# Optimization experiments

Measured on AMD Instinct MI355X. Metric: run time of the kernel, lower is better.

## Reference

```python
import jax, jax.numpy as jnp
import numpy as np

D = 64        # d_model = input_dims
S = 300       # patch_length
DFF = 256     # dff (H feature dim)
NH = 2        # num_heads
DK = D // NH  # 32


def _ln(x, g, b, eps=1e-5):
    m = x.mean(-1, keepdims=True)
    v = ((x - m) ** 2).mean(-1, keepdims=True)
    return (x - m) * jax.lax.rsqrt(v + eps) * g + b


def setup_inputs() -> dict:
    key = jax.random.key(0)
    ks = jax.random.split(key, 20)
    B = 256
    inp = {
        "state": jax.random.normal(ks[0], (B, S, D), dtype=jnp.float32),
        "H": jax.random.normal(ks[1], (B, S, DFF), dtype=jnp.float32),
    }
    # Linear weights stored as [in, out] (torch stores [out, in]; math is x @ W_in_out + b)
    def lin(k, din, dout):
        k1, k2 = jax.random.split(k)
        w = jax.random.normal(k1, (din, dout), dtype=jnp.float32) / np.sqrt(din)
        b = jax.random.normal(k2, (dout,), dtype=jnp.float32) * 0.01
        return w, b
    inp["Wq"], inp["bq"] = lin(ks[2], D, D)
    inp["Wk"], inp["bk"] = lin(ks[3], D, D)
    inp["Wv"], inp["bv"] = lin(ks[4], D, D)
    inp["Wcq"], inp["bcq"] = lin(ks[5], DFF, D)
    inp["Wck"], inp["bck"] = lin(ks[6], DFF, D)
    inp["Wcv"], inp["bcv"] = lin(ks[7], DFF, D)
    # six LayerNorms on d_model (QE/KE/VE from state branch, QH/KH/VH from H branch)
    for name in ["QE", "KE", "VE", "QH", "KH", "VH"]:
        inp[f"g{name}"] = jnp.ones((D,), jnp.float32)
        inp[f"beta{name}"] = jnp.zeros((D,), jnp.float32)
    inp["W1"], inp["b1"] = lin(ks[8], D, 4 * D)
    inp["W2"], inp["b2"] = lin(ks[9], 4 * D, D)
    inp["g1"] = jnp.ones((D,), jnp.float32)   # norm1
    inp["beta1"] = jnp.zeros((D,), jnp.float32)
    return inp


def reference(state, H, Wq, bq, Wk, bk, Wv, bv, Wcq, bcq, Wck, bck, Wcv, bcv,
              gQE, betaQE, gKE, betaKE, gVE, betaVE,
              gQH, betaQH, gKH, betaKH, gVH, betaVH,
              W1, b1, W2, b2, g1, beta1):
    B = state.shape[0]
    # gated q/k/v: LN(Linear(state)) * LN(Linear(H)), split into heads
    def branch(Wx, bx, gx, bbx, Wh, bh, gh, bbh):
        e = _ln(state @ Wx + bx, gx, bbx)
        h = _ln(H @ Wh + bh, gh, bbh)
        return (e * h).reshape(B, S, NH, DK).transpose(0, 2, 1, 3)  # [B,NH,S,DK]
    q = branch(Wq, bq, gQE, betaQE, Wcq, bcq, gQH, betaQH)
    k = branch(Wk, bk, gKE, betaKE, Wck, bck, gKH, betaKH)
    v = branch(Wv, bv, gVE, betaVE, Wcv, bcv, gVH, betaVH)
    scores = jnp.einsum("bhqd,bhkd->bhqk", q, k) / jnp.sqrt(jnp.float32(DK))
    attn = jax.nn.softmax(scores, axis=-1)
    out = jnp.einsum("bhqk,bhkd->bhqd", attn, v)
    out = out.transpose(0, 2, 1, 3).reshape(B, S, NH * DK)
    Z1 = state + out                      # dropout p=0.01 -> identity in eval
    Z2 = _ln(Z1, g1, beta1)
    Z3 = jax.nn.gelu(Z2 @ W1 + b1, approximate=False)  # torch F.gelu default = exact erf
    Z4 = Z3 @ W2 + b2
    return Z1 + Z4
```

## Files before the change

### kernel.cpp

```cpp
#include <hip/hip_runtime.h>
#include <math.h>

namespace {

constexpr int SEQ  = 300;
constexpr int DM   = 64;
constexpr int DFFN = 256;
constexpr int NBAT = 256;
constexpr int ROWS = NBAT * SEQ;
constexpr float EPS = 1e-5f;

typedef __attribute__((ext_vector_type(8))) short s16x8;
typedef __attribute__((ext_vector_type(4))) float f32x4;

__device__ __forceinline__ float4 ld4(const float* p) { return *reinterpret_cast<const float4*>(p); }

__device__ __forceinline__ ushort f2bf(float x) {
  unsigned u = __builtin_bit_cast(unsigned, x);
  u += 0x7FFFu + ((u >> 16) & 1u);
  return (ushort)(u >> 16);
}

struct PrepArgs {
  const float *Wq,*Wk,*Wv,*Wcq,*Wck,*Wcv;
  const float *bq,*bk,*bv,*bcq,*bck,*bcv;
  const float *gQE,*betaQE,*gKE,*betaKE,*gVE,*betaVE;
  const float *gQH,*betaQH,*gKH,*betaKH,*gVH,*betaVH;
  const float *W1,*W2;
  ushort *Bqkv, *W1t, *W2t;
  float *pk;
};

__global__ __launch_bounds__(256) void tb_prep(PrepArgs P) {
  const int idx = blockIdx.x * 256 + threadIdx.x;
  if (idx < 61440) {
    const int c = idx / 12288, rem = idx % 12288;
    const int n = rem >> 6, k = rem & 63;
    const int br = n >> 6, col = n & 63;
    float v;
    if (c == 0) {
      const float* W = (br == 0) ? P.Wq : (br == 1) ? P.Wk : P.Wv;
      v = W[k * DM + col];
    } else {
      const float* W = (br == 0) ? P.Wcq : (br == 1) ? P.Wck : P.Wcv;
      v = W[((c - 1) * 64 + k) * DM + col];
    }
    P.Bqkv[c * 12288 + ((n * 128 + ((k * 2) ^ ((n & 7) << 4))) >> 1)] = f2bf(v);
  } else if (idx < 77824) {
    const int r = idx - 61440, n = r >> 6, k = r & 63;
    P.W1t[(n * 128 + ((k * 2) ^ ((n & 7) << 4))) >> 1] = f2bf(P.W1[k * DFFN + n]);
  } else if (idx < 94208) {
    const int j = idx - 77824;
    const int fragId = j >> 9, within = j & 511;
    const int lane = within >> 3, e = within & 7;
    const int ps = fragId >> 2, nt2 = fragId & 3;
    const int n = nt2 * 16 + (lane & 15);
    const int k = ps * 32 + ((e >> 2) << 4) + ((lane >> 4) << 2) + (e & 3);
    P.W2t[j] = f2bf(P.W2[k * DM + n]);
  } else if (idx < 95360) {
    const int r = idx - 94208, which = r / 192, j = r % 192;
    const int br = j >> 6, col = j & 63;
    const float* s;
    switch (which) {
      case 0:  s = (br==0)?P.bq   :(br==1)?P.bk    :P.bv;     break;
      case 1:  s = (br==0)?P.bcq  :(br==1)?P.bck   :P.bcv;    break;
      case 2:  s = (br==0)?P.gQE  :(br==1)?P.gKE   :P.gVE;    break;
      case 3:  s = (br==0)?P.betaQE:(br==1)?P.betaKE:P.betaVE; break;
      case 4:  s = (br==0)?P.gQH  :(br==1)?P.gKH   :P.gVH;    break;
      default: s = (br==0)?P.betaQH:(br==1)?P.betaKH:P.betaVH; break;
    }
    P.pk[which * 192 + j] = s[col];
  }
}

struct QkvArgs {
  const float *state, *H;
  const ushort *Bqkv;
  const float *pk;
  ushort *qo, *ko, *vo;
};

__global__ __launch_bounds__(256) void tb_qkv(QkvArgs A) {
  __shared__ __align__(16) ushort Ab[4608];
  __shared__ __align__(16) ushort Bb[12288];
  const int t = threadIdx.x;
  const int lane = t & 63, w = t >> 6;
  const int lo = lane & 15, hi = lane >> 4;
  const int rowbase = blockIdx.x * 64;

  f32x4 accE[12], accH[12];
  #pragma unroll
  for (int nt = 0; nt < 12; ++nt) {
    const float bE = A.pk[nt * 16 + lo], bH = A.pk[192 + nt * 16 + lo];
    accE[nt] = (f32x4){bE, bE, bE, bE};
    accH[nt] = (f32x4){bH, bH, bH, bH};
  }

  const int arow = w * 16 + lo;
  const int aswz = (lo & 7) << 4;

#define STAGE_B(c)                                                            \
  _Pragma("unroll")                                                           \
  for (int i = 0; i < 6; ++i) {                                               \
    const int s_ = i * 256 + t;                                               \
    *(uint4*)&Bb[s_ * 8] = *(const uint4*)&A.Bqkv[(c) * 12288 + s_ * 8];      \
  }

#define STAGE_A(SRC, STRIDE)                                                  \
  _Pragma("unroll")                                                           \
  for (int i = 0; i < 4; ++i) {                                               \
    const int p_ = i * 256 + t;                                               \
    const int row_ = p_ >> 4, slot_ = p_ & 15;                                \
    const float4 f_ = ld4(&(SRC)[row_ * (STRIDE) + slot_ * 4]);               \
    ushort4 u_;                                                               \
    u_.x = f2bf(f_.x); u_.y = f2bf(f_.y); u_.z = f2bf(f_.z); u_.w = f2bf(f_.w);\
    *(ushort4*)((char*)Ab + (row_ * 128 + ((slot_ * 8) ^ ((row_ & 7) << 4)))) = u_; \
  }

#define COMPUTE(ACC)                                                          \
  _Pragma("unroll")                                                           \
  for (int ks = 0; ks < 2; ++ks) {                                            \
    const s16x8 af = *(const s16x8*)((const char*)Ab +                        \
        (arow * 128 + ((ks * 64 + hi * 16) ^ aswz)));                         \
    _Pragma("unroll")                                                         \
    for (int nt = 0; nt < 12; ++nt) {                                         \
      const int n_ = nt * 16 + lo;                                            \
      const s16x8 bf = *(const s16x8*)((const char*)Bb +                      \
          (n_ * 128 + ((ks * 64 + hi * 16) ^ ((n_ & 7) << 4))));              \
      ACC[nt] = __builtin_amdgcn_mfma_f32_16x16x32_bf16(af, bf, ACC[nt], 0, 0, 0); \
    }                                                                         \
  }

  STAGE_B(0)
  STAGE_A(A.state + (size_t)rowbase * 64, 64)
  __syncthreads();
  COMPUTE(accE)
  for (int c = 1; c < 5; ++c) {
    __syncthreads();
    STAGE_B(c)
    const float* hsrc = A.H + (size_t)rowbase * 256 + (c - 1) * 64;
    STAGE_A(hsrc, 256)
    __syncthreads();
    COMPUTE(accH)
  }
#undef STAGE_B
#undef STAGE_A
#undef COMPUTE

  const float* gE  = A.pk + 384;
  const float* bEt = A.pk + 576;
  const float* gH  = A.pk + 768;
  const float* bHt = A.pk + 960;
  const int growbase = rowbase + w * 16 + hi * 4;
  float vout[4][4];

  #pragma unroll
  for (int br = 0; br < 3; ++br) {
    #pragma unroll
    for (int r = 0; r < 4; ++r) {
      float s1 = 0.f, s2 = 0.f, u1 = 0.f, u2 = 0.f;
      #pragma unroll
      for (int qq = 0; qq < 4; ++qq) {
        const float ev = accE[br * 4 + qq][r], hv = accH[br * 4 + qq][r];
        s1 += ev; s2 += ev * ev; u1 += hv; u2 += hv * hv;
      }
      #pragma unroll
      for (int m = 1; m <= 8; m <<= 1) {
        s1 += __shfl_xor(s1, m, 64); s2 += __shfl_xor(s2, m, 64);
        u1 += __shfl_xor(u1, m, 64); u2 += __shfl_xor(u2, m, 64);
      }
      const float me = s1 * (1.f / 64.f);
      const float re = rsqrtf(s2 * (1.f / 64.f) - me * me + EPS);
      const float mh = u1 * (1.f / 64.f);
      const float rh = rsqrtf(u2 * (1.f / 64.f) - mh * mh + EPS);
      const int grow = growbase + r;
      const int bb = grow / 300, ss = grow - bb * 300;
      #pragma unroll
      for (int qq = 0; qq < 4; ++qq) {
        const int colg = (br * 4 + qq) * 16 + lo;
        const float en = (accE[br * 4 + qq][r] - me) * re * gE[colg] + bEt[colg];
        const float hn = (accH[br * 4 + qq][r] - mh) * rh * gH[colg] + bHt[colg];
        const float val = en * hn;
        if (br == 2) {
          vout[r][qq] = val;
        } else {
          const int cb = qq * 16 + lo;
          const int hh = cb >> 5, dk = cb & 31;
          ushort* dst = (br == 0) ? A.qo : A.ko;
          const float sc = (br == 0) ? 0.17677669529663687f : 1.f;
          dst[((size_t)(bb * 2 + hh) * 300 + ss) * 32 + dk] = f2bf(val * sc);
        }
      }
    }
  }

  __syncthreads();
  ushort* vbuf = Ab;
  #pragma unroll
  for (int r = 0; r < 4; ++r) {
    const int sl = w * 16 + hi * 4 + r;
    #pragma unroll
    for (int qq = 0; qq < 4; ++qq) {
      const int dk = qq * 16 + lo;
      vbuf[dk * 68 + sl] = f2bf(vout[r][qq]);
    }
  }
  __syncthreads();
  #pragma unroll
  for (int i = 0; i < 4; ++i) {
    const int p = i * 256 + t;
    const int dk = p >> 4, sg = p & 15;
    const int grow = rowbase + sg * 4;
    const int bb = grow / 300, ss = grow - bb * 300;
    const int hh = dk >> 5, dkh = dk & 31;
    ushort4 val;
    val.x = vbuf[dk * 68 + sg * 4 + 0];
    val.y = vbuf[dk * 68 + sg * 4 + 1];
    val.z = vbuf[dk * 68 + sg * 4 + 2];
    val.w = vbuf[dk * 68 + sg * 4 + 3];
    *(ushort4*)&A.vo[(size_t)(bb * 2 + hh) * 9600 + dkh * 300 + ss] = val;
  }
}

__global__ __launch_bounds__(256, 2) void tb_attn(const ushort* __restrict__ q,
    const ushort* __restrict__ k, const ushort* __restrict__ vt, float* __restrict__ ao)
{
  __shared__ __align__(16) char lk[304 * 64];
  __shared__ __align__(16) char lv[32 * 656];

  const int t = threadIdx.x;
  const int hh = blockIdx.x, b = blockIdx.y;
  const size_t bh = (size_t)(b * 2 + hh);

  const char* qg = (const char*)(q + bh * 300 * 32);
  const char* kg = (const char*)(k + bh * 300 * 32);
  const char* vg = (const char*)(vt + bh * 32 * 300);

  for (int c = t; c < 1216; c += 256) {
    const int lin = c * 16;
    const int row = c >> 2;
    uint4 val = make_uint4(0u, 0u, 0u, 0u);
    if (row < 300) val = *(const uint4*)(kg + lin);
    *(uint4*)(lk + (lin ^ ((lin >> 2) & 0x70))) = val;
  }
  for (int i = t; i < 320; i += 256) {
    const int row = i / 10, cc = i - row * 10;
    *(unsigned*)(lv + row * 656 + 600 + cc * 4) = 0u;
  }
  for (int i = t; i < 2400; i += 256) {
    const int row = i / 75, cc = i - row * 75;
    *(uint2*)(lv + row * 656 + cc * 8) = *(const uint2*)(vg + row * 600 + cc * 8);
  }
  __syncthreads();

  const int lane = t & 63, wid = t >> 6;
  const int lo = lane & 15, hi = lane >> 4;
  const f32x4 zero = {0.f, 0.f, 0.f, 0.f};

  for (int qt = wid; qt < 19; qt += 4) {
    const int qrow = qt * 16 + lo;
    s16x8 qf = __builtin_bit_cast(s16x8, make_uint4(0u, 0u, 0u, 0u));
    if (qrow < 300) qf = *(const s16x8*)(qg + qrow * 64 + hi * 16);

    f32x4 p[19];
    #pragma unroll
    for (int kt = 0; kt < 19; ++kt) {
      int ka = (kt * 16 + lo) * 64 + hi * 16;
      ka ^= (ka >> 2) & 0x70;
      const s16x8 kf = *(const s16x8*)(lk + ka);
      p[kt] = __builtin_amdgcn_mfma_f32_16x16x32_bf16(kf, qf, zero, 0, 0, 0);
    }

    float mx = -1e30f;
    #pragma unroll
    for (int kt = 0; kt < 19; ++kt)
      #pragma unroll
      for (int r = 0; r < 4; ++r) mx = fmaxf(mx, p[kt][r]);
    mx = fmaxf(mx, __shfl_xor(mx, 16, 64));
    mx = fmaxf(mx, __shfl_xor(mx, 32, 64));

    #pragma unroll
    for (int kt = 0; kt < 19; ++kt)
      #pragma unroll
      for (int r = 0; r < 4; ++r) p[kt][r] = __expf(p[kt][r] - mx);
    if (hi == 3) p[18] = zero;

    float sum = 0.f;
    #pragma unroll
    for (int kt = 0; kt < 19; ++kt)
      #pragma unroll
      for (int r = 0; r < 4; ++r) sum += p[kt][r];
    sum += __shfl_xor(sum, 16, 64);
    sum += __shfl_xor(sum, 32, 64);
    const float inv = 1.f / sum;

    s16x8 pb[10];
    #pragma unroll
    for (int pr = 0; pr < 9; ++pr) {
      uint4 wv;
      wv.x = (unsigned)f2bf(p[2*pr][0] * inv)   | ((unsigned)f2bf(p[2*pr][1] * inv) << 16);
      wv.y = (unsigned)f2bf(p[2*pr][2] * inv)   | ((unsigned)f2bf(p[2*pr][3] * inv) << 16);
      wv.z = (unsigned)f2bf(p[2*pr+1][0] * inv) | ((unsigned)f2bf(p[2*pr+1][1] * inv) << 16);
      wv.w = (unsigned)f2bf(p[2*pr+1][2] * inv) | ((unsigned)f2bf(p[2*pr+1][3] * inv) << 16);
      pb[pr] = __builtin_bit_cast(s16x8, wv);
    }
    {
      uint4 wv;
      wv.x = (unsigned)f2bf(p[18][0] * inv) | ((unsigned)f2bf(p[18][1] * inv) << 16);
      wv.y = (unsigned)f2bf(p[18][2] * inv) | ((unsigned)f2bf(p[18][3] * inv) << 16);
      wv.z = 0u; wv.w = 0u;
      pb[9] = __builtin_bit_cast(s16x8, wv);
    }

    f32x4 acc0 = zero, acc1 = zero;
    #pragma unroll
    for (int pr = 0; pr < 10; ++pr) {
      const int byte0 = pr * 64 + hi * 8;
      uint4 w0, w1;
      {
        const uint2 a = *(const uint2*)(lv + lo * 656 + byte0);
        const uint2 c = *(const uint2*)(lv + lo * 656 + byte0 + 32);
        w0.x = a.x; w0.y = a.y; w0.z = c.x; w0.w = c.y;
      }
      {
        const uint2 a = *(const uint2*)(lv + (lo + 16) * 656 + byte0);
        const uint2 c = *(const uint2*)(lv + (lo + 16) * 656 + byte0 + 32);
        w1.x = a.x; w1.y = a.y; w1.z = c.x; w1.w = c.y;
      }
      acc0 = __builtin_amdgcn_mfma_f32_16x16x32_bf16(pb[pr], __builtin_bit_cast(s16x8, w0), acc0, 0, 0, 0);
      acc1 = __builtin_amdgcn_mfma_f32_16x16x32_bf16(pb[pr], __builtin_bit_cast(s16x8, w1), acc1, 0, 0, 0);
    }

    float* aop = ao + ((size_t)b * 300) * 64 + hh * 32;
    const int s0 = qt * 16 + hi * 4;
    #pragma unroll
    for (int r = 0; r < 4; ++r) {
      const int s = s0 + r;
      if (s < 300) {
        aop[s * 64 + lo]      = acc0[r];
        aop[s * 64 + 16 + lo] = acc1[r];
      }
    }
  }
}

struct FfnArgs {
  const float *state, *ao;
  const ushort *W1t, *W2t;
  const float *b1, *b2, *g1, *beta1;
  float* out;
};

__global__ __launch_bounds__(256) void tb_ffn(FfnArgs F) {
  __shared__ __align__(16) ushort Z2b[4096];
  __shared__ __align__(16) ushort Wb[16384];
  const int t = threadIdx.x;
  const int lane = t & 63, w = t >> 6;
  const int lo = lane & 15, hi = lane >> 4;
  const int rowbase = blockIdx.x * 64;

  #pragma unroll
  for (int i = 0; i < 8; ++i) {
    const int s_ = i * 256 + t;
    *(uint4*)&Wb[s_ * 8] = *(const uint4*)&F.W1t[s_ * 8];
  }

  {
    const int lrow = t >> 2;
    const int lcg  = (t & 3) * 16;
    const size_t gb = (size_t)(rowbase + lrow) * 64 + lcg;
    float xv[16];
    #pragma unroll
    for (int i = 0; i < 4; ++i) {
      const float4 a = ld4(&F.state[gb + i * 4]);
      const float4 b = ld4(&F.ao[gb + i * 4]);
      xv[i*4+0] = a.x + b.x; xv[i*4+1] = a.y + b.y;
      xv[i*4+2] = a.z + b.z; xv[i*4+3] = a.w + b.w;
    }
    float s1 = 0.f, s2 = 0.f;
    #pragma unroll
    for (int j = 0; j < 16; ++j) { s1 += xv[j]; s2 += xv[j] * xv[j]; }
    s1 += __shfl_xor(s1, 1, 64); s2 += __shfl_xor(s2, 1, 64);
    s1 += __shfl_xor(s1, 2, 64); s2 += __shfl_xor(s2, 2, 64);
    const float mean = s1 * (1.f / 64.f);
    const float rstd = rsqrtf(s2 * (1.f / 64.f) - mean * mean + EPS);
    float gv[16], bv[16];
    #pragma unroll
    for (int i = 0; i < 4; ++i) {
      *(float4*)&gv[i*4] = ld4(&F.g1[lcg + i * 4]);
      *(float4*)&bv[i*4] = ld4(&F.beta1[lcg + i * 4]);
    }
    #pragma unroll
    for (int h = 0; h < 2; ++h) {
      float z[8];
      #pragma unroll
      for (int j = 0; j < 8; ++j)
        z[j] = (xv[h*8+j] - mean) * rstd * gv[h*8+j] + bv[h*8+j];
      uint4 pkd;
      pkd.x = (unsigned)f2bf(z[0]) | ((unsigned)f2bf(z[1]) << 16);
      pkd.y = (unsigned)f2bf(z[2]) | ((unsigned)f2bf(z[3]) << 16);
      pkd.z = (unsigned)f2bf(z[4]) | ((unsigned)f2bf(z[5]) << 16);
      pkd.w = (unsigned)f2bf(z[6]) | ((unsigned)f2bf(z[7]) << 16);
      *(uint4*)((char*)Z2b + (lrow * 128 + (((lcg + h * 8) * 2) ^ ((lrow & 7) << 4)))) = pkd;
    }
  }
  __syncthreads();

  const int arow = w * 16 + lo;
  const int aswz = (lo & 7) << 4;

  s16x8 zf0, zf1;
  zf0 = *(const s16x8*)((const char*)Z2b + (arow * 128 + ((0 * 64 + hi * 16) ^ aswz)));
  zf1 = *(const s16x8*)((const char*)Z2b + (arow * 128 + ((1 * 64 + hi * 16) ^ aswz)));

  s16x8 pz[8];
  #pragma unroll
  for (int ps = 0; ps < 8; ++ps) {
    const int n0 = (2 * ps) * 16, n1 = (2 * ps + 1) * 16;
    const float4 bb0 = ld4(&F.b1[n0 + hi * 4]);
    const float4 bb1 = ld4(&F.b1[n1 + hi * 4]);
    f32x4 a0 = (f32x4){bb0.x, bb0.y, bb0.z, bb0.w};
    f32x4 a1 = (f32x4){bb1.x, bb1.y, bb1.z, bb1.w};
    #pragma unroll
    for (int ks = 0; ks < 2; ++ks) {
      const s16x8 zf = ks ? zf1 : zf0;
      const int na = n0 + lo, nb = n1 + lo;
      const s16x8 wfa = *(const s16x8*)((const char*)Wb + (na * 128 + ((ks * 64 + hi * 16) ^ ((na & 7) << 4))));
      const s16x8 wfb = *(const s16x8*)((const char*)Wb + (nb * 128 + ((ks * 64 + hi * 16) ^ ((nb & 7) << 4))));
      a0 = __builtin_amdgcn_mfma_f32_16x16x32_bf16(wfa, zf, a0, 0, 0, 0);
      a1 = __builtin_amdgcn_mfma_f32_16x16x32_bf16(wfb, zf, a1, 0, 0, 0);
    }
    float ga[8];
    #pragma unroll
    for (int e = 0; e < 8; ++e) {
      const float xg = (e < 4) ? a0[e & 3] : a1[e & 3];
      ga[e] = 0.5f * xg * (1.f + erff(xg * 0.70710678118654752f));
    }
    uint4 wv;
    wv.x = (unsigned)f2bf(ga[0]) | ((unsigned)f2bf(ga[1]) << 16);
    wv.y = (unsigned)f2bf(ga[2]) | ((unsigned)f2bf(ga[3]) << 16);
    wv.z = (unsigned)f2bf(ga[4]) | ((unsigned)f2bf(ga[5]) << 16);
    wv.w = (unsigned)f2bf(ga[6]) | ((unsigned)f2bf(ga[7]) << 16);
    pz[ps] = __builtin_bit_cast(s16x8, wv);
  }
  __syncthreads();

  #pragma unroll
  for (int i = 0; i < 8; ++i) {
    const int s_ = i * 256 + t;
    *(uint4*)&Wb[s_ * 8] = *(const uint4*)&F.W2t[s_ * 8];
  }
  __syncthreads();

  f32x4 acc2[4];
  #pragma unroll
  for (int nt = 0; nt < 4; ++nt) { const float b = F.b2[nt * 16 + lo]; acc2[nt] = (f32x4){b, b, b, b}; }
  #pragma unroll
  for (int ps = 0; ps < 8; ++ps) {
    #pragma unroll
    for (int nt = 0; nt < 4; ++nt) {
      const s16x8 bf = *(const s16x8*)&Wb[((ps * 4 + nt) * 64 + lane) * 8];
      acc2[nt] = __builtin_amdgcn_mfma_f32_16x16x32_bf16(pz[ps], bf, acc2[nt], 0, 0, 0);
    }
  }

  #pragma unroll
  for (int nt = 0; nt < 4; ++nt) {
    #pragma unroll
    for (int r = 0; r < 4; ++r) {
      const int grow = rowbase + w * 16 + hi * 4 + r;
      const int col = nt * 16 + lo;
      const size_t gidx = (size_t)grow * 64 + col;
      const float z1 = F.state[gidx] + F.ao[gidx];
      F.out[gidx] = z1 + acc2[nt][r];
    }
  }
}

}

extern "C" void kernel_launch(void* const* d_in, const int* in_sizes, int n_in,
                              void* d_out, int out_size, void* d_ws, size_t ws_size,
                              hipStream_t stream)
{
  const float* state = (const float*)d_in[0];
  const float* H     = (const float*)d_in[1];
  const float* Wq  = (const float*)d_in[2];  const float* bq  = (const float*)d_in[3];
  const float* Wk  = (const float*)d_in[4];  const float* bk  = (const float*)d_in[5];
  const float* Wv  = (const float*)d_in[6];  const float* bv  = (const float*)d_in[7];
  const float* Wcq = (const float*)d_in[8];  const float* bcq = (const float*)d_in[9];
  const float* Wck = (const float*)d_in[10]; const float* bck = (const float*)d_in[11];
  const float* Wcv = (const float*)d_in[12]; const float* bcv = (const float*)d_in[13];
  const float* gQE = (const float*)d_in[14]; const float* betaQE = (const float*)d_in[15];
  const float* gKE = (const float*)d_in[16]; const float* betaKE = (const float*)d_in[17];
  const float* gVE = (const float*)d_in[18]; const float* betaVE = (const float*)d_in[19];
  const float* gQH = (const float*)d_in[20]; const float* betaQH = (const float*)d_in[21];
  const float* gKH = (const float*)d_in[22]; const float* betaKH = (const float*)d_in[23];
  const float* gVH = (const float*)d_in[24]; const float* betaVH = (const float*)d_in[25];
  const float* W1 = (const float*)d_in[26]; const float* b1 = (const float*)d_in[27];
  const float* W2 = (const float*)d_in[28]; const float* b2 = (const float*)d_in[29];
  const float* g1 = (const float*)d_in[30]; const float* beta1 = (const float*)d_in[31];

  constexpr size_t QKV_E = (size_t)NBAT * 2 * 300 * 32;
  float*  ao_ws = (float*)d_ws;
  ushort* q_ws  = (ushort*)(ao_ws + (size_t)ROWS * DM);
  ushort* k_ws  = q_ws + QKV_E;
  ushort* v_ws  = k_ws + QKV_E;
  ushort* Bqkv  = v_ws + QKV_E;
  ushort* W1t   = Bqkv + 61440;
  ushort* W2t   = W1t + 16384;
  float*  pk    = (float*)(W2t + 16384);

  PrepArgs P;
  P.Wq = Wq; P.Wk = Wk; P.Wv = Wv; P.Wcq = Wcq; P.Wck = Wck; P.Wcv = Wcv;
  P.bq = bq; P.bk = bk; P.bv = bv; P.bcq = bcq; P.bck = bck; P.bcv = bcv;
  P.gQE = gQE; P.betaQE = betaQE; P.gKE = gKE; P.betaKE = betaKE;
  P.gVE = gVE; P.betaVE = betaVE; P.gQH = gQH; P.betaQH = betaQH;
  P.gKH = gKH; P.betaKH = betaKH; P.gVH = gVH; P.betaVH = betaVH;
  P.W1 = W1; P.W2 = W2;
  P.Bqkv = Bqkv; P.W1t = W1t; P.W2t = W2t; P.pk = pk;
  tb_prep<<<373, 256, 0, stream>>>(P);

  QkvArgs A;
  A.state = state; A.H = H; A.Bqkv = Bqkv; A.pk = pk;
  A.qo = q_ws; A.ko = k_ws; A.vo = v_ws;
  tb_qkv<<<ROWS / 64, 256, 0, stream>>>(A);

  tb_attn<<<dim3(2, NBAT), 256, 0, stream>>>(q_ws, k_ws, v_ws, ao_ws);

  FfnArgs F;
  F.state = state; F.ao = ao_ws; F.W1t = W1t; F.W2t = W2t;
  F.b1 = b1; F.b2 = b2; F.g1 = g1; F.beta1 = beta1; F.out = (float*)d_out;
  tb_ffn<<<ROWS / 64, 256, 0, stream>>>(F);
}
```

Measured before the change: 126.8 us.

## Load A fragments directly to registers and double-buffer weight tiles in QKV kernel

Each lane now loads its A-operand rows of state/H straight from global memory into registers and converts them to bf16 there, so the A tile no longer goes through shared memory. The weight (B) tiles are double-buffered in LDS, and the next chunk is staged while the current chunk's MFMAs run, which drops one barrier per iteration. This is meant to cut LDS traffic and barrier stalls. In exchange, each lane issues strided 32-byte global loads that may coalesce less well, and shared-memory use grows to two B buffers, which could lower occupancy.

```diff
diff --git a/kernel.cpp b/kernel.cpp
--- a/kernel.cpp
+++ b/kernel.cpp
@@ -81,8 +81,7 @@
 };
 
 __global__ __launch_bounds__(256) void tb_qkv(QkvArgs A) {
-  __shared__ __align__(16) ushort Ab[4608];
-  __shared__ __align__(16) ushort Bb[12288];
+  __shared__ __align__(16) ushort Bb[2][12288];
   const int t = threadIdx.x;
   const int lane = t & 63, w = t >> 6;
   const int lo = lane & 15, hi = lane >> 4;
@@ -96,56 +95,59 @@
     accH[nt] = (f32x4){bH, bH, bH, bH};
   }
 
-  const int arow = w * 16 + lo;
-  const int aswz = (lo & 7) << 4;
-
-#define STAGE_B(c)                                                            \
+  const int arowg = rowbase + w * 16 + lo;
+  const float* stp = A.state + (size_t)arowg * 64;
+  const float* hp  = A.H + (size_t)arowg * 256;
+
+#define STAGE_B(c, buf)                                                       \
   _Pragma("unroll")                                                           \
   for (int i = 0; i < 6; ++i) {                                               \
     const int s_ = i * 256 + t;                                               \
-    *(uint4*)&Bb[s_ * 8] = *(const uint4*)&A.Bqkv[(c) * 12288 + s_ * 8];      \
-  }
-
-#define STAGE_A(SRC, STRIDE)                                                  \
-  _Pragma("unroll")                                                           \
-  for (int i = 0; i < 4; ++i) {                                               \
-    const int p_ = i * 256 + t;                                               \
-    const int row_ = p_ >> 4, slot_ = p_ & 15;                                \
-    const float4 f_ = ld4(&(SRC)[row_ * (STRIDE) + slot_ * 4]);               \
-    ushort4 u_;                                                               \
-    u_.x = f2bf(f_.x); u_.y = f2bf(f_.y); u_.z = f2bf(f_.z); u_.w = f2bf(f_.w);\
-    *(ushort4*)((char*)Ab + (row_ * 128 + ((slot_ * 8) ^ ((row_ & 7) << 4)))) = u_; \
-  }
-
-#define COMPUTE(ACC)                                                          \
-  _Pragma("unroll")                                                           \
-  for (int ks = 0; ks < 2; ++ks) {                                            \
-    const s16x8 af = *(const s16x8*)((const char*)Ab +                        \
-        (arow * 128 + ((ks * 64 + hi * 16) ^ aswz)));                         \
-    _Pragma("unroll")                                                         \
-    for (int nt = 0; nt < 12; ++nt) {                                         \
-      const int n_ = nt * 16 + lo;                                            \
-      const s16x8 bf = *(const s16x8*)((const char*)Bb +                      \
-          (n_ * 128 + ((ks * 64 + hi * 16) ^ ((n_ & 7) << 4))));              \
-      ACC[nt] = __builtin_amdgcn_mfma_f32_16x16x32_bf16(af, bf, ACC[nt], 0, 0, 0); \
-    }                                                                         \
-  }
-
-  STAGE_B(0)
-  STAGE_A(A.state + (size_t)rowbase * 64, 64)
-  __syncthreads();
-  COMPUTE(accE)
-  for (int c = 1; c < 5; ++c) {
+    *(uint4*)&Bb[buf][s_ * 8] = *(const uint4*)&A.Bqkv[(c) * 12288 + s_ * 8]; \
+  }
+
+  STAGE_B(0, 0)
+  __syncthreads();
+
+  #pragma unroll
+  for (int c = 0; c < 5; ++c) {
+    const int cur = c & 1;
+    const float* ap = (c == 0) ? stp : (hp + (c - 1) * 64);
+    const float4 a0 = ld4(ap + hi * 8);
+    const float4 a1 = ld4(ap + hi * 8 + 4);
+    const float4 a2 = ld4(ap + 32 + hi * 8);
+    const float4 a3 = ld4(ap + 32 + hi * 8 + 4);
+    if (c < 4) { STAGE_B(c + 1, cur ^ 1) }
+    struct S8 { ushort4 a, b; } p0, p1;
+    p0.a.x = f2bf(a0.x); p0.a.y = f2bf(a0.y); p0.a.z = f2bf(a0.z); p0.a.w = f2bf(a0.w);
+    p0.b.x = f2bf(a1.x); p0.b.y = f2bf(a1.y); p0.b.z = f2bf(a1.z); p0.b.w = f2bf(a1.w);
+    p1.a.x = f2bf(a2.x); p1.a.y = f2bf(a2.y); p1.a.z = f2bf(a2.z); p1.a.w = f2bf(a2.w);
+    p1.b.x = f2bf(a3.x); p1.b.y = f2bf(a3.y); p1.b.z = f2bf(a3.z); p1.b.w = f2bf(a3.w);
+    const s16x8 af0 = __builtin_bit_cast(s16x8, p0);
+    const s16x8 af1 = __builtin_bit_cast(s16x8, p1);
+    const char* bbase = (const char*)&Bb[cur][0];
+    if (c == 0) {
+      #pragma unroll
+      for (int nt = 0; nt < 12; ++nt) {
+        const int n_ = nt * 16 + lo;
+        const s16x8 bf0 = *(const s16x8*)(bbase + (n_ * 128 + ((hi * 16) ^ ((n_ & 7) << 4))));
+        accE[nt] = __builtin_amdgcn_mfma_f32_16x16x32_bf16(af0, bf0, accE[nt], 0, 0, 0);
+        const s16x8 bf1 = *(const s16x8*)(bbase + (n_ * 128 + ((64 + hi * 16) ^ ((n_ & 7) << 4))));
+        accE[nt] = __builtin_amdgcn_mfma_f32_16x16x32_bf16(af1, bf1, accE[nt], 0, 0, 0);
+      }
+    } else {
+      #pragma unroll
+      for (int nt = 0; nt < 12; ++nt) {
+        const int n_ = nt * 16 + lo;
+        const s16x8 bf0 = *(const s16x8*)(bbase + (n_ * 128 + ((hi * 16) ^ ((n_ & 7) << 4))));
+        accH[nt] = __builtin_amdgcn_mfma_f32_16x16x32_bf16(af0, bf0, accH[nt], 0, 0, 0);
+        const s16x8 bf1 = *(const s16x8*)(bbase + (n_ * 128 + ((64 + hi * 16) ^ ((n_ & 7) << 4))));
+        accH[nt] = __builtin_amdgcn_mfma_f32_16x16x32_bf16(af1, bf1, accH[nt], 0, 0, 0);
+      }
+    }
     __syncthreads();
-    STAGE_B(c)
-    const float* hsrc = A.H + (size_t)rowbase * 256 + (c - 1) * 64;
-    STAGE_A(hsrc, 256)
-    __syncthreads();
-    COMPUTE(accH)
   }
 #undef STAGE_B
-#undef STAGE_A
-#undef COMPUTE
 
   const float* gE  = A.pk + 384;
   const float* bEt = A.pk + 576;
@@ -195,7 +197,7 @@
   }
 
   __syncthreads();
-  ushort* vbuf = Ab;
+  ushort* vbuf = &Bb[0][0];
   #pragma unroll
   for (int r = 0; r < 4; ++r) {
     const int sl = w * 16 + hi * 4 + r;
```

After: 132.6 us. 4.6% more time.
